# Kernel tuning notes

Measured on AMD Instinct MI355X. Metric: run time of the kernel, lower is better.

Reference implementation:

```python
import jax, jax.numpy as jnp
import numpy as np

RESET_PERIOD = 10
DECAY = 0.1
D_MODEL = 512
D_INNER = 1024
N_LAYERS = 4


def layer_norm(x, scale, bias, eps=1e-5):
    mu = jnp.mean(x, axis=-1, keepdims=True)
    var = jnp.mean((x - mu) ** 2, axis=-1, keepdims=True)
    return (x - mu) * jax.lax.rsqrt(var + eps) * scale + bias


def setup_inputs() -> dict:
    key = jax.random.key(0)
    ks = jax.random.split(key, 12)
    B, S, F, V, MF = 8, 2048, 128, 256, 4096
    D, DI, L = D_MODEL, D_INNER, N_LAYERS
    rn = lambda k, shape, s: jax.random.normal(k, shape, jnp.float32) * s
    return {
        "frames": rn(ks[0], (B, S, F), 1.0),
        "padding_mask": jax.random.uniform(ks[1], (B, S)) < 0.9,
        "W_in_proj": rn(ks[2], (F, D), 0.05),
        "b_in_proj": jnp.zeros((D,), jnp.float32),
        "pos_emb": rn(ks[3], (MF, D), 0.02),
        "ln_scale": jnp.ones((L, D), jnp.float32),
        "ln_bias": jnp.zeros((L, D), jnp.float32),
        "W_in": rn(ks[4], (L, D, 2 * DI), 0.03),
        "b_in": jnp.zeros((L, 2 * DI), jnp.float32),
        "W_out": rn(ks[5], (L, DI, D), 0.03),
        "b_out": jnp.zeros((L, D), jnp.float32),
        "fn_scale": jnp.ones((D,), jnp.float32),
        "fn_bias": jnp.zeros((D,), jnp.float32),
        "W_frame": rn(ks[6], (D, F), 0.03),
        "b_frame": jnp.zeros((F,), jnp.float32),
        "W_sym": rn(ks[7], (D, V), 0.03),
        "b_sym": jnp.zeros((V,), jnp.float32),
    }


def reference(frames, padding_mask, W_in_proj, b_in_proj, pos_emb,
              ln_scale, ln_bias, W_in, b_in, W_out, b_out,
              fn_scale, fn_bias, W_frame, b_frame, W_sym, b_sym):
    B, S, F = frames.shape
    # input projection + clamped positional embedding
    x = frames @ W_in_proj + b_in_proj                     # [B,S,D]
    pos = jnp.clip(jnp.arange(S), 0, pos_emb.shape[0] - 1)
    x = x + pos_emb[pos][None]
    # periodic hard-reset decay: frame_counter starts at 0, incremented AFTER
    # each step, so steps with (t+1) % reset_period == 0 are scaled.
    t = jnp.arange(S) + 1
    decay = jnp.where(t % RESET_PERIOD == 0, DECAY, 1.0)[None, :, None]  # [1,S,1]

    def layer(h, p):
        s, b, Wi, bi, Wo, bo = p
        n = layer_norm(h, s, b)
        uz = n @ Wi + bi                                   # [B,S,2*DI]
        u, g = jnp.split(uz, 2, axis=-1)
        y = (u * jax.nn.silu(g)) @ Wo + bo                 # [B,S,D]
        # wrapper scales the full block output (incl. residual)
        return (h + y) * decay, None

    x, _ = jax.lax.scan(layer, x, (ln_scale, ln_bias, W_in, b_in, W_out, b_out))
    x = layer_norm(x, fn_scale, fn_bias)
    frame_outputs = x @ W_frame + b_frame                  # [B,S,F]
    symbol_logits = x @ W_sym + b_sym                      # [B,S,V]
    m = padding_mask[..., None]
    frame_outputs = jnp.where(m, frame_outputs, 0.0)
    symbol_logits = jnp.where(m, symbol_logits, 0.0)
    return frame_outputs, symbol_logits
```

## Files before the change

kernel.cpp:

```cpp
#include <hip/hip_runtime.h>
#include <hip/hip_bf16.h>

using f32x4  = __attribute__((ext_vector_type(4))) float;
using bf16x8 = __attribute__((ext_vector_type(8))) short;
using bf16x4 = __attribute__((ext_vector_type(4))) short;

#define SEQ 2048

__device__ __forceinline__ short f2b(float f){
  unsigned u = __builtin_bit_cast(unsigned, f);
  u = (u + 0x7FFFu + ((u >> 16) & 1u)) >> 16;
  return (short)u;
}

__device__ __forceinline__ void gl_lds16(const short* g, short* l){
  __builtin_amdgcn_global_load_lds(
      (const __attribute__((address_space(1))) void*)g,
      (__attribute__((address_space(3))) void*)l, 16, 0, 0);
}

__device__ __forceinline__ bool mask_at(const void* mask, int flag, int m){
  if (flag == 1) return ((const unsigned char*)mask)[m] != 0;
  if (flag == 2) return ((const float*)mask)[m] != 0.0f;
  if (flag == 3) return ((const int*)mask)[2*m] != 0;
  return ((const int*)mask)[m] != 0;
}

__device__ __forceinline__ void tr32(float (*t)[33], const float* in, short* out,
                                     int R, int C, int bx, int by, int z, int glu){
  in  += (size_t)z * R * C;
  out += (size_t)z * R * C;
  int tx = threadIdx.x & 31, ty = threadIdx.x >> 5;
  int r0 = by * 32, c0 = bx * 32;
  #pragma unroll
  for (int i = 0; i < 4; i++)
    t[ty + i*8][tx] = in[(size_t)(r0 + ty + i*8) * C + c0 + tx];
  __syncthreads();
  #pragma unroll
  for (int i = 0; i < 4; i++){
    int oc = c0 + ty + i*8;
    int nr = oc;
    if (glu){
      int half = C >> 1;
      nr = (oc < half) ? (((oc >> 4) << 5) + (oc & 15))
                       : ((((oc - half) >> 4) << 5) + 16 + (oc & 15));
    }
    out[(size_t)nr * R + r0 + tx] = f2b(t[tx][ty + i*8]);
  }
}

__global__ __launch_bounds__(256) void prep(
    const float* __restrict__ frames, short* __restrict__ frb,
    const float* __restrict__ Wip, short* __restrict__ Wt0,
    const float* __restrict__ Win, short* __restrict__ Wt1,
    const float* __restrict__ Wout, short* __restrict__ Wt2,
    const float* __restrict__ Wfr, short* __restrict__ Wt3,
    const float* __restrict__ Wsy, short* __restrict__ Wt4,
    const unsigned char* __restrict__ mask, int* __restrict__ flag)
{
  __shared__ float t[32][33];
  const int b = blockIdx.x;
  if (b < 2048){
    int i = (b * 256 + threadIdx.x) * 4;
    float4 v = *(const float4*)(frames + i);
    bf16x4 o; o[0]=f2b(v.x); o[1]=f2b(v.y); o[2]=f2b(v.z); o[3]=f2b(v.w);
    *(bf16x4*)(frb + i) = o;
  } else if (b < 2112){
    int L = b - 2048; tr32(t, Wip, Wt0, 128, 512, L % 16, L / 16, 0, 0);
  } else if (b < 6208){
    int L = b - 2112; tr32(t, Win, Wt1, 512, 2048, L % 64, (L / 64) % 16, L / 1024, 1);
  } else if (b < 8256){
    int L = b - 6208; tr32(t, Wout, Wt2, 1024, 512, L % 16, (L / 16) % 32, L / 512, 0);
  } else if (b < 8320){
    int L = b - 8256; tr32(t, Wfr, Wt3, 512, 128, L % 4, L / 4, 0, 0);
  } else if (b < 8448){
    int L = b - 8320; tr32(t, Wsy, Wt4, 512, 256, L % 8, L / 8, 0, 0);
  } else {
    int* si = (int*)t;
    int tid = threadIdx.x;
    if (tid < 3) si[tid] = 0;
    __syncthreads();
    int ge2 = 0, off = 0, off8 = 0;
    for (int i = tid; i < 16384; i += 256){
      unsigned char c = mask[i];
      if (c >= 2) ge2++;
      if ((i & 3) && c) off++;
      if (((i & 7) == 4) && c) off8++;
    }
    atomicAdd(&si[0], ge2); atomicAdd(&si[1], off); atomicAdd(&si[2], off8);
    __syncthreads();
    if (tid == 0){
      int f;
      if      (si[0] > 0) f = 2;
      else if (si[1] > 0) f = 1;
      else if (si[2] > 0) f = 0;
      else                f = 3;
      *flag = f;
    }
  }
}

template<int K>
__global__ __launch_bounds__(512, 2) void glu8p(
    const short* __restrict__ A, const short* __restrict__ B,
    const float* __restrict__ bias, short* __restrict__ obuf)
{
  constexpr int NT = K / 64;
  constexpr int HT = NT * 4;
  __shared__ short lds[8 * 8192];

  const int nbx = gridDim.x;
  int bid = blockIdx.y * nbx + blockIdx.x;
  const int nwg = nbx * gridDim.y;
  bid = (bid & 7) * (nwg >> 3) + (bid >> 3);
  const int n0 = (bid % nbx) * 256, m0 = (bid / nbx) * 256;

  const int tid = threadIdx.x, lane = tid & 63, wid = tid >> 6;
  const int wr = wid >> 2, wc = wid & 3;
  const int fr = lane & 15, kg = lane >> 4;

  f32x4 acc[8][2][2];
  const f32x4 zero = {0.f, 0.f, 0.f, 0.f};
  #pragma unroll
  for (int i = 0; i < 8; i++)
    #pragma unroll
    for (int nh = 0; nh < 2; nh++)
      #pragma unroll
      for (int j = 0; j < 2; j++) acc[i][nh][j] = zero;

  const int rl0 = wid * 8 + (lane >> 3);
  const int swz = ((lane & 7) ^ ((lane >> 3) & 7)) * 8;
  const short* Ab = A + ((size_t)m0 + rl0) * K + swz;
  const short* Bb = B + ((size_t)n0 + rl0) * K + swz;

  auto stage = [&](int h){
    if (h < HT){
      const int q = h & 3, kt2 = h >> 2, slot = h & 7;
      const short* src = (q < 2) ? (Bb + (size_t)(q * 128) * K + kt2 * 64)
                                 : (Ab + (size_t)((q - 2) * 128) * K + kt2 * 64);
      short* dst = lds + slot * 8192 + wid * 512;
      gl_lds16(src, dst);
      gl_lds16(src + (size_t)64 * K, dst + 4096);
    }
  };

  #pragma unroll
  for (int h = 0; h < 5; h++) stage(h);
  asm volatile("s_waitcnt vmcnt(2)" ::: "memory");
  __builtin_amdgcn_s_barrier();

  for (int kt = 0; kt < NT; ++kt){
    bf16x8 aF[8];
    #pragma unroll
    for (int p = 0; p < 4; ++p){
      const int kb = p >> 1, nh = p & 1;
      const int ks = kg + kb * 4;
      if (nh == 0){
        const int slot = (4 * kt + 2 + wr) & 7;
        #pragma unroll
        for (int i = 0; i < 8; i++)
          aF[i] = *(const bf16x8*)((const char*)lds + slot * 16384
                     + (i * 16 + fr) * 128 + ((ks ^ (fr & 7)) * 16));
      }
      bf16x8 bF[2];
      {
        const int slot = (4 * kt + nh) & 7;
        #pragma unroll
        for (int j = 0; j < 2; j++)
          bF[j] = *(const bf16x8*)((const char*)lds + slot * 16384
                     + (wc * 32 + j * 16 + fr) * 128 + ((ks ^ (fr & 7)) * 16));
      }
      stage(4 * kt + p + 5);
      if (p == 3){
        if (kt < NT - 2)       asm volatile("s_waitcnt vmcnt(2)" ::: "memory");
        else if (kt == NT - 2) asm volatile("s_waitcnt vmcnt(0)" ::: "memory");
      }
      __builtin_amdgcn_s_barrier();
      __builtin_amdgcn_s_setprio(1);
      #pragma unroll
      for (int i = 0; i < 8; i++)
        #pragma unroll
        for (int j = 0; j < 2; j++)
          acc[i][nh][j] = __builtin_amdgcn_mfma_f32_16x16x32_bf16(aF[i], bF[j], acc[i][nh][j], 0, 0, 0);
      __builtin_amdgcn_s_setprio(0);
      __builtin_amdgcn_s_barrier();
    }
  }

  #pragma unroll
  for (int i = 0; i < 8; i++){
    #pragma unroll
    for (int nh = 0; nh < 2; nh++){
      const int pc = n0 + nh * 128 + wc * 32;
      const int lc = ((pc >> 5) << 4) + fr;
      #pragma unroll
      for (int r = 0; r < 4; r++){
        const int gm = m0 + wr * 128 + i * 16 + kg * 4 + r;
        float u = acc[i][nh][0][r] + bias[lc];
        float g = acc[i][nh][1][r] + bias[1024 + lc];
        float sg = g / (1.0f + expf(-g));
        obuf[(size_t)gm * 1024 + lc] = f2b(u * sg);
      }
    }
  }
}

template<int K>
__global__ __launch_bounds__(512, 2) void res8p(
    const short* __restrict__ A, const short* __restrict__ B,
    const float* __restrict__ bias,
    const float* __restrict__ sc, const float* __restrict__ bi,
    float* __restrict__ xbuf, short* __restrict__ nbuf)
{
  constexpr int NT = K / 64;
  __shared__ short lds[18 * 4096];

  int bid = blockIdx.x;
  const int nwg = gridDim.x;
  bid = (bid & 7) * (nwg >> 3) + (bid >> 3);
  const int m0 = bid * 64;

  const int tid = threadIdx.x, lane = tid & 63, wid = tid >> 6;
  const int fr = lane & 15, kg = lane >> 4;

  f32x4 acc[4][4];
  const f32x4 zero = {0.f, 0.f, 0.f, 0.f};
  #pragma unroll
  for (int i = 0; i < 4; i++)
    #pragma unroll
    for (int j = 0; j < 4; j++) acc[i][j] = zero;

  const int rl0 = tid >> 3;
  const int swz = ((tid & 7) ^ (rl0 & 7)) * 8;
  const short* Ab = A + ((size_t)m0 + rl0) * K + swz;
  const short* Bb = B + (size_t)rl0 * K + swz;

  auto stageT = [&](int t){
    if (t < NT){
      short* wb = lds + (t & 1) * 36864 + wid * 512;
      gl_lds16(Ab + t * 64, wb);
      #pragma unroll
      for (int u = 0; u < 8; u++)
        gl_lds16(Bb + (size_t)(u * 64) * K + t * 64, wb + (1 + u) * 4096);
    }
  };

  stageT(0);
  asm volatile("s_waitcnt vmcnt(0)" ::: "memory");
  __builtin_amdgcn_s_barrier();

  for (int kt = 0; kt < NT; ++kt){
    const char* buf = (const char*)lds + (kt & 1) * 73728;
    #pragma unroll
    for (int kb = 0; kb < 2; kb++){
      const int ks = kg + kb * 4;
      bf16x8 aF[4], bF[4];
      #pragma unroll
      for (int i = 0; i < 4; i++){
        const int row = i * 16 + fr;
        aF[i] = *(const bf16x8*)(buf + row * 128 + ((ks ^ (row & 7)) * 16));
      }
      #pragma unroll
      for (int j = 0; j < 4; j++){
        const int row = j * 16 + fr;
        bF[j] = *(const bf16x8*)(buf + (1 + wid) * 8192 + row * 128 + ((ks ^ (row & 7)) * 16));
      }
      if (kb == 0) stageT(kt + 1);
      else asm volatile("s_waitcnt vmcnt(0)" ::: "memory");
      __builtin_amdgcn_s_barrier();
      __builtin_amdgcn_s_setprio(1);
      #pragma unroll
      for (int i = 0; i < 4; i++)
        #pragma unroll
        for (int j = 0; j < 4; j++)
          acc[i][j] = __builtin_amdgcn_mfma_f32_16x16x32_bf16(aF[i], bF[j], acc[i][j], 0, 0, 0);
      __builtin_amdgcn_s_setprio(0);
      __builtin_amdgcn_s_barrier();
    }
  }

  #pragma unroll
  for (int i = 0; i < 4; i++){
    #pragma unroll
    for (int r = 0; r < 4; r++){
      const int row = i * 16 + kg * 4 + r;
      const int gm = m0 + row;
      const float d = ((((gm & (SEQ-1)) + 1) % 10) == 0) ? 0.1f : 1.0f;
      #pragma unroll
      for (int j = 0; j < 4; j++){
        const int gn = wid * 64 + j * 16 + fr;
        const float xo = xbuf[(size_t)gm * 512 + gn];
        acc[i][j][r] = (xo + acc[i][j][r] + bias[gn]) * d;
      }
    }
  }
  float* fs = (float*)lds;
  __syncthreads();
  #pragma unroll
  for (int i = 0; i < 4; i++){
    #pragma unroll
    for (int r = 0; r < 4; r++){
      float s = acc[i][0][r] + acc[i][1][r] + acc[i][2][r] + acc[i][3][r];
      float q = acc[i][0][r]*acc[i][0][r] + acc[i][1][r]*acc[i][1][r]
              + acc[i][2][r]*acc[i][2][r] + acc[i][3][r]*acc[i][3][r];
      #pragma unroll
      for (int o = 1; o < 16; o <<= 1){ s += __shfl_xor(s, o); q += __shfl_xor(q, o); }
      if (fr == 0){
        const int row = i * 16 + kg * 4 + r;
        fs[wid * 64 + row]       = s;
        fs[512 + wid * 64 + row] = q;
      }
    }
  }
  __syncthreads();
  if (tid < 64){
    float s = 0.f, q = 0.f;
    #pragma unroll
    for (int w8 = 0; w8 < 8; w8++){ s += fs[w8 * 64 + tid]; q += fs[512 + w8 * 64 + tid]; }
    const float mu = s * (1.0f / 512.0f);
    const float var = q * (1.0f / 512.0f) - mu * mu;
    fs[1024 + tid] = mu;
    fs[1088 + tid] = rsqrtf(var + 1e-5f);
  }
  __syncthreads();
  #pragma unroll
  for (int i = 0; i < 4; i++){
    #pragma unroll
    for (int r = 0; r < 4; r++){
      const int row = i * 16 + kg * 4 + r;
      const int gm = m0 + row;
      const float mu = fs[1024 + row], rs = fs[1088 + row];
      #pragma unroll
      for (int j = 0; j < 4; j++){
        const int gn = wid * 64 + j * 16 + fr;
        const float v = acc[i][j][r];
        xbuf[(size_t)gm * 512 + gn] = v;
        nbuf[(size_t)gm * 512 + gn] = f2b((v - mu) * rs * sc[gn] + bi[gn]);
      }
    }
  }
}

__global__ __launch_bounds__(512, 2) void in0ln(
    const short* __restrict__ A, const short* __restrict__ B,
    const float* __restrict__ bias, const float* __restrict__ pos,
    const float* __restrict__ sc, const float* __restrict__ bi,
    float* __restrict__ xbuf, short* __restrict__ nbuf)
{
  constexpr int K = 128;
  __shared__ short lds[18 * 4096];

  int bid = blockIdx.x;
  const int nwg = gridDim.x;
  bid = (bid & 7) * (nwg >> 3) + (bid >> 3);
  const int m0 = bid * 64;

  const int tid = threadIdx.x, lane = tid & 63, wid = tid >> 6;
  const int fr = lane & 15, kg = lane >> 4;

  f32x4 acc[4][4];
  const f32x4 zero = {0.f, 0.f, 0.f, 0.f};
  #pragma unroll
  for (int i = 0; i < 4; i++)
    #pragma unroll
    for (int j = 0; j < 4; j++) acc[i][j] = zero;

  const int rl0 = tid >> 3;
  const int swz = ((tid & 7) ^ (rl0 & 7)) * 8;
  const short* Ab = A + ((size_t)m0 + rl0) * K + swz;
  const short* Bb = B + (size_t)rl0 * K + swz;

  #pragma unroll
  for (int t = 0; t < 2; t++){
    short* wb = lds + t * 36864 + wid * 512;
    gl_lds16(Ab + t * 64, wb);
    #pragma unroll
    for (int u = 0; u < 8; u++)
      gl_lds16(Bb + (size_t)(u * 64) * K + t * 64, wb + (1 + u) * 4096);
  }
  asm volatile("s_waitcnt vmcnt(0)" ::: "memory");
  __builtin_amdgcn_s_barrier();

  #pragma unroll
  for (int kt = 0; kt < 2; ++kt){
    const char* buf = (const char*)lds + kt * 73728;
    #pragma unroll
    for (int kb = 0; kb < 2; kb++){
      const int ks = kg + kb * 4;
      bf16x8 aF[4], bF[4];
      #pragma unroll
      for (int i = 0; i < 4; i++){
        const int row = i * 16 + fr;
        aF[i] = *(const bf16x8*)(buf + row * 128 + ((ks ^ (row & 7)) * 16));
      }
      #pragma unroll
      for (int j = 0; j < 4; j++){
        const int row = j * 16 + fr;
        bF[j] = *(const bf16x8*)(buf + (1 + wid) * 8192 + row * 128 + ((ks ^ (row & 7)) * 16));
      }
      #pragma unroll
      for (int i = 0; i < 4; i++)
        #pragma unroll
        for (int j = 0; j < 4; j++)
          acc[i][j] = __builtin_amdgcn_mfma_f32_16x16x32_bf16(aF[i], bF[j], acc[i][j], 0, 0, 0);
    }
  }

  #pragma unroll
  for (int i = 0; i < 4; i++){
    #pragma unroll
    for (int r = 0; r < 4; r++){
      const int row = i * 16 + kg * 4 + r;
      const int gm = m0 + row;
      #pragma unroll
      for (int j = 0; j < 4; j++){
        const int gn = wid * 64 + j * 16 + fr;
        acc[i][j][r] += bias[gn] + pos[(size_t)(gm & (SEQ-1)) * 512 + gn];
      }
    }
  }
  float* fs = (float*)lds;
  __syncthreads();
  #pragma unroll
  for (int i = 0; i < 4; i++){
    #pragma unroll
    for (int r = 0; r < 4; r++){
      float s = acc[i][0][r] + acc[i][1][r] + acc[i][2][r] + acc[i][3][r];
      float q = acc[i][0][r]*acc[i][0][r] + acc[i][1][r]*acc[i][1][r]
              + acc[i][2][r]*acc[i][2][r] + acc[i][3][r]*acc[i][3][r];
      #pragma unroll
      for (int o = 1; o < 16; o <<= 1){ s += __shfl_xor(s, o); q += __shfl_xor(q, o); }
      if (fr == 0){
        const int row = i * 16 + kg * 4 + r;
        fs[wid * 64 + row]       = s;
        fs[512 + wid * 64 + row] = q;
      }
    }
  }
  __syncthreads();
  if (tid < 64){
    float s = 0.f, q = 0.f;
    #pragma unroll
    for (int w8 = 0; w8 < 8; w8++){ s += fs[w8 * 64 + tid]; q += fs[512 + w8 * 64 + tid]; }
    const float mu = s * (1.0f / 512.0f);
    const float var = q * (1.0f / 512.0f) - mu * mu;
    fs[1024 + tid] = mu;
    fs[1088 + tid] = rsqrtf(var + 1e-5f);
  }
  __syncthreads();
  #pragma unroll
  for (int i = 0; i < 4; i++){
    #pragma unroll
    for (int r = 0; r < 4; r++){
      const int row = i * 16 + kg * 4 + r;
      const int gm = m0 + row;
      const float mu = fs[1024 + row], rs = fs[1088 + row];
      #pragma unroll
      for (int j = 0; j < 4; j++){
        const int gn = wid * 64 + j * 16 + fr;
        const float v = acc[i][j][r];
        xbuf[(size_t)gm * 512 + gn] = v;
        nbuf[(size_t)gm * 512 + gn] = f2b((v - mu) * rs * sc[gn] + bi[gn]);
      }
    }
  }
}

__global__ __launch_bounds__(256) void heads_k(
    const short* __restrict__ A, const short* __restrict__ B,
    const float* __restrict__ bias0, const float* __restrict__ bias1,
    float* __restrict__ fout, const void* __restrict__ mask, const int* __restrict__ flagp)
{
  constexpr int K = 512, BM = 128, BN = 128;
  __shared__ short lds[(BM + BN) * 64];
  short* lA = lds;
  short* lB = lds + BM * 64;

  const int nbx = gridDim.x;
  int bid = blockIdx.y * nbx + blockIdx.x;
  const int nwg = nbx * gridDim.y;
  bid = (bid & 7) * (nwg >> 3) + (bid >> 3);
  const int n0 = (bid % nbx) * BN, m0 = (bid / nbx) * BM;

  const int tid = threadIdx.x, lane = tid & 63, wid = tid >> 6;
  const int lr  = lane >> 3;
  const int lks = (lane & 7) ^ (lr & 7);
  const int fr = lane & 15;
  const int kg = lane >> 4;

  const int wr = wid >> 1, wc = wid & 1;
  const int rA0 = wr * 64 + fr;
  const int rB0 = wc * 64 + fr;

  f32x4 acc[4][4];
  const f32x4 zero = {0.f, 0.f, 0.f, 0.f};
  #pragma unroll
  for (int i = 0; i < 4; i++)
    #pragma unroll
    for (int j = 0; j < 4; j++) acc[i][j] = zero;

  const short* Ab = A + (size_t)m0 * K + (size_t)lr * K + lks * 8;
  const short* Bb = B + (size_t)n0 * K + (size_t)lr * K + lks * 8;

  for (int kt = 0; kt < K; kt += 64){
    __syncthreads();
    #pragma unroll
    for (int c = 0; c < 4; c++)
      gl_lds16(Ab + kt + (size_t)(wid + c * 4) * 8 * K, lA + (wid + c * 4) * 512);
    #pragma unroll
    for (int c = 0; c < 4; c++)
      gl_lds16(Bb + kt + (size_t)(wid + c * 4) * 8 * K, lB + (wid + c * 4) * 512);
    __syncthreads();

    #pragma unroll
    for (int kb8 = 0; kb8 < 8; kb8 += 4){
      bf16x8 aF[4], bF[4];
      #pragma unroll
      for (int i = 0; i < 4; i++){
        const int row = rA0 + i * 16;
        aF[i] = *(const bf16x8*)((const char*)lA + row * 128 + (((kg + kb8) ^ (row & 7)) * 16));
      }
      #pragma unroll
      for (int j = 0; j < 4; j++){
        const int row = rB0 + j * 16;
        bF[j] = *(const bf16x8*)((const char*)lB + row * 128 + (((kg + kb8) ^ (row & 7)) * 16));
      }
      #pragma unroll
      for (int i = 0; i < 4; i++)
        #pragma unroll
        for (int j = 0; j < 4; j++)
          acc[i][j] = __builtin_amdgcn_mfma_f32_16x16x32_bf16(aF[i], bF[j], acc[i][j], 0, 0, 0);
    }
  }

  const int col0 = n0 + wc * 64 + fr;
  const int row0 = m0 + wr * 64 + kg * 4;
  const int flag = *flagp;

  #pragma unroll
  for (int i = 0; i < 4; i++){
    #pragma unroll
    for (int r = 0; r < 4; r++){
      const int gm = row0 + i * 16 + r;
      const bool mk = mask_at(mask, flag, gm);
      #pragma unroll
      for (int j = 0; j < 4; j++){
        const int gn = col0 + j * 16;
        const float v = acc[i][j][r];
        if (gn < 128){
          fout[(size_t)gm * 128 + gn] = mk ? (v + bias0[gn]) : 0.0f;
        } else {
          const int gs = gn - 128;
          fout[(size_t)16384 * 128 + (size_t)gm * 256 + gs] = mk ? (v + bias1[gs]) : 0.0f;
        }
      }
    }
  }
}

extern "C" void kernel_launch(void* const* d_in, const int* in_sizes, int n_in,
                              void* d_out, int out_size, void* d_ws, size_t ws_size,
                              hipStream_t stream){
  const float* frames    = (const float*)d_in[0];
  const void*  mask      = d_in[1];
  const float* W_in_proj = (const float*)d_in[2];
  const float* b_in_proj = (const float*)d_in[3];
  const float* pos_emb   = (const float*)d_in[4];
  const float* ln_scale  = (const float*)d_in[5];
  const float* ln_bias   = (const float*)d_in[6];
  const float* W_in      = (const float*)d_in[7];
  const float* b_in      = (const float*)d_in[8];
  const float* W_out     = (const float*)d_in[9];
  const float* b_out     = (const float*)d_in[10];
  const float* fn_scale  = (const float*)d_in[11];
  const float* fn_bias   = (const float*)d_in[12];
  const float* W_frame   = (const float*)d_in[13];
  const float* b_frame   = (const float*)d_in[14];
  const float* W_sym     = (const float*)d_in[15];
  const float* b_sym     = (const float*)d_in[16];

  char* w = (char*)d_ws;
  int*   flag = (int*)w;
  float* xbuf = (float*)(w + 256);
  short* nbuf = (short*)(w + 256 + 33554432);
  short* abuf = (short*)(w + 256 + 33554432 + 16777216);
  short* frb  = (short*)(w + 256 + 33554432 + 16777216 + 33554432);
  short* Wt0  = frb + (size_t)16384 * 128;
  short* Wt1  = Wt0 + (size_t)512 * 128;
  short* Wt2  = Wt1 + (size_t)4 * 2048 * 512;
  short* Wt3  = Wt2 + (size_t)4 * 512 * 1024;
  short* Wt4  = Wt3 + (size_t)128 * 512;

  prep<<<8449, 256, 0, stream>>>(frames, frb, W_in_proj, Wt0, W_in, Wt1, W_out, Wt2,
                                 W_frame, Wt3, W_sym, Wt4, (const unsigned char*)mask, flag);

  in0ln<<<256, 512, 0, stream>>>(frb, Wt0, b_in_proj, pos_emb, ln_scale, ln_bias, xbuf, nbuf);

  for (int l = 0; l < 4; l++){
    glu8p<512><<<dim3(8, 64), 512, 0, stream>>>(nbuf,
        Wt1 + (size_t)l * 2048 * 512, b_in + l * 2048, abuf);
    const float* s2 = (l < 3) ? (ln_scale + (l + 1) * 512) : fn_scale;
    const float* b2 = (l < 3) ? (ln_bias  + (l + 1) * 512) : fn_bias;
    res8p<1024><<<256, 512, 0, stream>>>(abuf, Wt2 + (size_t)l * 512 * 1024,
        b_out + l * 512, s2, b2, xbuf, nbuf);
  }

  heads_k<<<dim3(3, 128), 256, 0, stream>>>(nbuf, Wt3, b_frame, b_sym,
      (float*)d_out, mask, flag);
}
```

Before: 514.2 us.

## Deepen LDS prefetch pipelines in GLU and output-projection GEMM kernels

The GLU GEMM moves from an 8-slot to a 9-slot LDS ring buffer with 7 stages in flight instead of 5. The stage order is changed to A first, then B, and both k-halves of the A fragments are kept in registers so each A tile is read once per k-step. The second GEMM issues the next tile's loads earlier, one tile further ahead and after the mid-iteration barrier, so more global-load latency overlaps with MFMA work. The cost is more LDS and registers, which may hurt occupancy, and in the second kernel a load may now be issued into a buffer before all waves have finished reading it.

Measured after the change: 510.2 us. About the same (-0.8%).

```diff
diff --git a/kernel.cpp b/kernel.cpp
--- a/kernel.cpp
+++ b/kernel.cpp
@@ -107,7 +107,7 @@
 {
   constexpr int NT = K / 64;
   constexpr int HT = NT * 4;
-  __shared__ short lds[8 * 8192];
+  __shared__ short lds[9 * 8192];
 
   const int nbx = gridDim.x;
   int bid = blockIdx.y * nbx + blockIdx.x;
@@ -133,58 +133,78 @@
   const short* Ab = A + ((size_t)m0 + rl0) * K + swz;
   const short* Bb = B + ((size_t)n0 + rl0) * K + swz;
 
-  auto stage = [&](int h){
+  auto stage = [&](int h, int slot){
     if (h < HT){
-      const int q = h & 3, kt2 = h >> 2, slot = h & 7;
-      const short* src = (q < 2) ? (Bb + (size_t)(q * 128) * K + kt2 * 64)
-                                 : (Ab + (size_t)((q - 2) * 128) * K + kt2 * 64);
+      const int q = h & 3, kt2 = h >> 2;
+      const short* src = (q < 2) ? (Ab + (size_t)(q * 128) * K + kt2 * 64)
+                                 : (Bb + (size_t)((q - 2) * 128) * K + kt2 * 64);
       short* dst = lds + slot * 8192 + wid * 512;
       gl_lds16(src, dst);
       gl_lds16(src + (size_t)64 * K, dst + 4096);
     }
   };
 
-  #pragma unroll
-  for (int h = 0; h < 5; h++) stage(h);
-  asm volatile("s_waitcnt vmcnt(2)" ::: "memory");
+  int ss = 0;
+  #pragma unroll
+  for (int h = 0; h < 7; h++){ stage(h, ss); ss++; }
+  asm volatile("s_waitcnt vmcnt(6)" ::: "memory");
   __builtin_amdgcn_s_barrier();
 
+  int rb = 0;
   for (int kt = 0; kt < NT; ++kt){
-    bf16x8 aF[8];
+    int sA = rb + wr;  if (sA >= 9) sA -= 9;
+    int sB0 = rb + 2;  if (sB0 >= 9) sB0 -= 9;
+    int sB1 = rb + 3;  if (sB1 >= 9) sB1 -= 9;
+    bf16x8 aF0[8], aF1[8];
     #pragma unroll
     for (int p = 0; p < 4; ++p){
-      const int kb = p >> 1, nh = p & 1;
+      const int nh = p >> 1, kb = p & 1;
       const int ks = kg + kb * 4;
-      if (nh == 0){
-        const int slot = (4 * kt + 2 + wr) & 7;
+      if (p == 0){
         #pragma unroll
         for (int i = 0; i < 8; i++)
-          aF[i] = *(const bf16x8*)((const char*)lds + slot * 16384
-                     + (i * 16 + fr) * 128 + ((ks ^ (fr & 7)) * 16));
+          aF0[i] = *(const bf16x8*)((const char*)lds + sA * 16384
+                     + (i * 16 + fr) * 128 + ((kg ^ (fr & 7)) * 16));
+      }
+      if (p == 1){
+        #pragma unroll
+        for (int i = 0; i < 8; i++)
+          aF1[i] = *(const bf16x8*)((const char*)lds + sA * 16384
+                     + (i * 16 + fr) * 128 + (((kg + 4) ^ (fr & 7)) * 16));
       }
       bf16x8 bF[2];
       {
-        const int slot = (4 * kt + nh) & 7;
+        const int sB = (nh == 0) ? sB0 : sB1;
         #pragma unroll
         for (int j = 0; j < 2; j++)
-          bF[j] = *(const bf16x8*)((const char*)lds + slot * 16384
+          bF[j] = *(const bf16x8*)((const char*)lds + sB * 16384
                      + (wc * 32 + j * 16 + fr) * 128 + ((ks ^ (fr & 7)) * 16));
       }
-      stage(4 * kt + p + 5);
+      stage(4 * kt + p + 7, ss);
+      ss++; if (ss == 9) ss = 0;
       if (p == 3){
-        if (kt < NT - 2)       asm volatile("s_waitcnt vmcnt(2)" ::: "memory");
+        if (kt < NT - 2)       asm volatile("s_waitcnt vmcnt(6)" ::: "memory");
         else if (kt == NT - 2) asm volatile("s_waitcnt vmcnt(0)" ::: "memory");
       }
       __builtin_amdgcn_s_barrier();
       __builtin_amdgcn_s_setprio(1);
-      #pragma unroll
-      for (int i = 0; i < 8; i++)
-        #pragma unroll
-        for (int j = 0; j < 2; j++)
-          acc[i][nh][j] = __builtin_amdgcn_mfma_f32_16x16x32_bf16(aF[i], bF[j], acc[i][nh][j], 0, 0, 0);
+      if (kb == 0){
+        #pragma unroll
+        for (int i = 0; i < 8; i++)
+          #pragma unroll
+          for (int j = 0; j < 2; j++)
+            acc[i][nh][j] = __builtin_amdgcn_mfma_f32_16x16x32_bf16(aF0[i], bF[j], acc[i][nh][j], 0, 0, 0);
+      } else {
+        #pragma unroll
+        for (int i = 0; i < 8; i++)
+          #pragma unroll
+          for (int j = 0; j < 2; j++)
+            acc[i][nh][j] = __builtin_amdgcn_mfma_f32_16x16x32_bf16(aF1[i], bF[j], acc[i][nh][j], 0, 0, 0);
+      }
       __builtin_amdgcn_s_setprio(0);
       __builtin_amdgcn_s_barrier();
     }
+    rb += 4; if (rb >= 9) rb -= 9;
   }
 
   #pragma unroll
@@ -248,12 +268,34 @@
   stageT(0);
   asm volatile("s_waitcnt vmcnt(0)" ::: "memory");
   __builtin_amdgcn_s_barrier();
+  stageT(1);
 
   for (int kt = 0; kt < NT; ++kt){
     const char* buf = (const char*)lds + (kt & 1) * 73728;
-    #pragma unroll
-    for (int kb = 0; kb < 2; kb++){
-      const int ks = kg + kb * 4;
+    {
+      bf16x8 aF[4], bF[4];
+      #pragma unroll
+      for (int i = 0; i < 4; i++){
+        const int row = i * 16 + fr;
+        aF[i] = *(const bf16x8*)(buf + row * 128 + ((kg ^ (row & 7)) * 16));
+      }
+      #pragma unroll
+      for (int j = 0; j < 4; j++){
+        const int row = j * 16 + fr;
+        bF[j] = *(const bf16x8*)(buf + (1 + wid) * 8192 + row * 128 + ((kg ^ (row & 7)) * 16));
+      }
+      __builtin_amdgcn_s_barrier();
+      __builtin_amdgcn_s_setprio(1);
+      #pragma unroll
+      for (int i = 0; i < 4; i++)
+        #pragma unroll
+        for (int j = 0; j < 4; j++)
+          acc[i][j] = __builtin_amdgcn_mfma_f32_16x16x32_bf16(aF[i], bF[j], acc[i][j], 0, 0, 0);
+      __builtin_amdgcn_s_setprio(0);
+      __builtin_amdgcn_s_barrier();
+    }
+    {
+      const int ks = kg + 4;
       bf16x8 aF[4], bF[4];
       #pragma unroll
       for (int i = 0; i < 4; i++){
@@ -265,9 +307,9 @@
         const int row = j * 16 + fr;
         bF[j] = *(const bf16x8*)(buf + (1 + wid) * 8192 + row * 128 + ((ks ^ (row & 7)) * 16));
       }
-      if (kb == 0) stageT(kt + 1);
-      else asm volatile("s_waitcnt vmcnt(0)" ::: "memory");
+      if (kt < NT - 1) asm volatile("s_waitcnt vmcnt(0)" ::: "memory");
       __builtin_amdgcn_s_barrier();
+      stageT(kt + 2);
       __builtin_amdgcn_s_setprio(1);
       #pragma unroll
       for (int i = 0; i < 4; i++)
```
